# Optimization experiments

Hardware: AMD Instinct MI355X
Metric: run time of the kernel (lower is better)

## Reference

```python
import jax, jax.numpy as jnp
import numpy as np

H = 16          # num_heads
EPS = 1e-6      # RMSNorm eps


def setup_inputs() -> dict:
    key = jax.random.key(0)
    ks = jax.random.split(key, 5)
    B, N, D = 4, 4096, 1024
    x = jax.random.normal(ks[0], (B, N, D), dtype=jnp.float32)
    q = jax.random.normal(ks[1], (D,), dtype=jnp.float32)
    k = jax.random.normal(ks[2], (D,), dtype=jnp.float32)
    log_decay = jax.random.normal(ks[3], (H,), dtype=jnp.float32)
    norm_weight = jnp.ones((D,), dtype=jnp.float32)
    o_w = jax.random.normal(ks[4], (D, D), dtype=jnp.float32) * 0.02
    return {"x": x, "q": q, "k": k, "log_decay": log_decay,
            "norm_weight": norm_weight, "o_w": o_w}


def reference(x, q, k, log_decay, norm_weight, o_w):
    b, n, dm = x.shape
    dh = dm // H
    qh = q.reshape(H, dh)            # per-head query vector (constant over b, n)
    kh = k.reshape(H, dh)            # per-head key vector
    v = x.reshape(b, n, H, dh)       # values = input tokens
    # exp(logsigmoid(a)) == sigmoid(a): per-head decay in (0, 1)
    lam = jax.nn.sigmoid(log_decay)  # (H,)

    def step(S, v_t):
        # S: (b, H, dh, dh) recurrent state;  v_t: (b, H, dh)
        S = lam[None, :, None, None] * S + kh[None, :, :, None] * v_t[:, :, None, :]
        o_t = jnp.einsum('hd,bhdv->bhv', qh, S)
        return S, o_t

    S0 = jnp.zeros((b, H, dh, dh), dtype=x.dtype)
    _, o = jax.lax.scan(step, S0, jnp.moveaxis(v, 1, 0))  # o: (n, b, H, dh)
    o = jnp.moveaxis(o, 0, 1).reshape(b, n, dm)

    # RMSNorm over the channel dim
    o = o * jax.lax.rsqrt(jnp.mean(o * o, axis=-1, keepdims=True) + EPS) * norm_weight
    # o_proj (no bias)
    return o @ o_w.T
```

## Files before the change

kernel.cpp:

```cpp
#include <hip/hip_runtime.h>
#include <hip/hip_bf16.h>
#include <cstdint>
#include <cstddef>

#define HH   16
#define BB   4
#define NN   4096
#define DD   1024
#define MM   (BB * NN)
#define NC   128
#define LC   32
#define EPSV 1e-6f

typedef short short8 __attribute__((ext_vector_type(8)));
typedef float floatx4 __attribute__((ext_vector_type(4)));

__device__ __forceinline__ void async_copy16(const void* g, void* l) {
    __builtin_amdgcn_global_load_lds(
        (const __attribute__((address_space(1))) void*)g,
        (__attribute__((address_space(3))) void*)l, 16, 0, 0);
}

__device__ __forceinline__ uint2 pack_bf16x4(float a, float b, float c, float d) {
    union { __hip_bfloat16 h[4]; uint2 u; } cv;
    cv.h[0] = __float2bfloat16(a); cv.h[1] = __float2bfloat16(b);
    cv.h[2] = __float2bfloat16(c); cv.h[3] = __float2bfloat16(d);
    return cv.u;
}

__device__ __forceinline__ float sigmoidf(float a) {
    return 1.f / (1.f + expf(-a));
}

__global__ void k_wconv(const float* __restrict__ ow, const float* __restrict__ nw,
                        __hip_bfloat16* __restrict__ wp) {
    size_t i4 = (size_t)blockIdx.x * 256 + threadIdx.x;
    int j = (int)((i4 * 4) & (DD - 1));
    float4 v = ((const float4*)ow)[i4];
    ((uint2*)wp)[i4] = pack_bf16x4(v.x * nw[j], v.y * nw[j + 1],
                                   v.z * nw[j + 2], v.w * nw[j + 3]);
}

__global__ void k_chunk_end(const float* __restrict__ x, const float* __restrict__ ld,
                            float* __restrict__ E) {
    int b = blockIdx.x >> 7, c = blockIdx.x & (NC - 1);
    int j4 = threadIdx.x;
    float lam = sigmoidf(ld[j4 >> 4]);
    const float4* xp = (const float4*)(x + ((size_t)(b * NN + c * LC)) * DD) + j4;
    float4 e = {0.f, 0.f, 0.f, 0.f};
    #pragma unroll
    for (int t = 0; t < LC; ++t) {
        float4 v = xp[(size_t)t * (DD / 4)];
        e.x = fmaf(lam, e.x, v.x); e.y = fmaf(lam, e.y, v.y);
        e.z = fmaf(lam, e.z, v.z); e.w = fmaf(lam, e.w, v.w);
    }
    ((float4*)(E + (size_t)blockIdx.x * DD))[j4] = e;
}

__global__ void k_carry(const float* __restrict__ ld, const float* __restrict__ E,
                        float* __restrict__ P) {
    __shared__ float tile[NC][33];
    int b = blockIdx.x >> 5, jg = blockIdx.x & 31;
    int tid = threadIdx.x;
    int cc = tid >> 5, jj = tid & 31;
    #pragma unroll
    for (int it = 0; it < 16; ++it) {
        int c = it * 8 + cc;
        tile[c][jj] = E[(size_t)(b * NC + c) * DD + jg * 32 + jj];
    }
    __syncthreads();
    if (tid < 32) {
        int j = jg * 32 + tid;
        float lam = sigmoidf(ld[j >> 6]);
        float lamL = lam;
        lamL *= lamL; lamL *= lamL; lamL *= lamL; lamL *= lamL; lamL *= lamL;
        float p = 0.f;
        for (int c = 0; c < NC; ++c) {
            float e = tile[c][tid];
            tile[c][tid] = p;
            p = fmaf(lamL, p, e);
        }
    }
    __syncthreads();
    #pragma unroll
    for (int it = 0; it < 16; ++it) {
        int c = it * 8 + cc;
        P[(size_t)(b * NC + c) * DD + jg * 32 + jj] = tile[c][jj];
    }
}

__global__ void k_scan(const float* __restrict__ x, const float* __restrict__ q,
                       const float* __restrict__ k, const float* __restrict__ ld,
                       const float* __restrict__ P, __hip_bfloat16* __restrict__ obf,
                       float* __restrict__ sumsq) {
    __shared__ float ssq[4][LC];
    int b = blockIdx.x >> 7, c = blockIdx.x & (NC - 1);
    int j4 = threadIdx.x;
    int h = j4 >> 4;
    float lam = sigmoidf(ld[h]);
    float4 q4 = ((const float4*)q)[j4];
    float4 k4 = ((const float4*)k)[j4];
    float ch = q4.x * k4.x + q4.y * k4.y + q4.z * k4.z + q4.w * k4.w;
    #pragma unroll
    for (int off = 1; off < 16; off <<= 1) ch += __shfl_xor(ch, off);
    int row0 = b * NN + c * LC;
    int lane = threadIdx.x & 63, w = threadIdx.x >> 6;
    const float4* xp = (const float4*)(x + (size_t)row0 * DD) + j4;
    float4 y = ((const float4*)(P + (size_t)blockIdx.x * DD))[j4];
    for (int t = 0; t < LC; ++t) {
        float4 v = xp[(size_t)t * (DD / 4)];
        y.x = fmaf(lam, y.x, v.x); y.y = fmaf(lam, y.y, v.y);
        y.z = fmaf(lam, y.z, v.z); y.w = fmaf(lam, y.w, v.w);
        float ox = ch * y.x, oy = ch * y.y, oz = ch * y.z, ow = ch * y.w;
        ((uint2*)(obf + (size_t)(row0 + t) * DD))[j4] = pack_bf16x4(ox, oy, oz, ow);
        float s = ox * ox + oy * oy + oz * oz + ow * ow;
        #pragma unroll
        for (int off = 32; off > 0; off >>= 1) s += __shfl_xor(s, off);
        if (lane == 0) ssq[w][t] = s;
    }
    __syncthreads();
    if (threadIdx.x < LC) {
        int t = threadIdx.x;
        sumsq[row0 + t] = ssq[0][t] + ssq[1][t] + ssq[2][t] + ssq[3][t];
    }
}

#define GEMM_STAGE(SLOT, S)                                                    \
  do {                                                                         \
    char* _da = (char*)&lds[SLOT][0][0] + w * 1024;                            \
    char* _db = (char*)&lds[SLOT][1][0] + w * 1024;                            \
    _Pragma("unroll") for (int _i = 0; _i < 2; ++_i)                           \
      async_copy16(Ag + (size_t)(m0 + _i * 128 + rr) * 1024 + (S) * 32 + oo * 8, \
                   _da + _i * 8192);                                           \
    _Pragma("unroll") for (int _i = 0; _i < 2; ++_i)                           \
      async_copy16(Wg + (size_t)(n0 + _i * 128 + rr) * 1024 + (S) * 32 + oo * 8, \
                   _db + _i * 8192);                                           \
  } while (0)

#define GEMM_CONSUME(SLOT)                                                     \
  do {                                                                         \
    short8 af[8]; short8 bf[4];                                                \
    const short* _a = &lds[SLOT][0][0];                                        \
    const short* _b = &lds[SLOT][1][0];                                        \
    _Pragma("unroll") for (int mt = 0; mt < 8; ++mt)                           \
      af[mt] = *(const short8*)(_a + (arow_base + mt * 16) * 32 + p_rd * 8);   \
    _Pragma("unroll") for (int nt = 0; nt < 4; ++nt)                           \
      bf[nt] = *(const short8*)(_b + (brow_base + nt * 16) * 32 + p_rd * 8);   \
    asm volatile("s_waitcnt lgkmcnt(0)" ::: "memory");                         \
    __builtin_amdgcn_s_setprio(1);                                             \
    _Pragma("unroll") for (int mt = 0; mt < 8; ++mt) {                         \
      _Pragma("unroll") for (int nt = 0; nt < 4; ++nt)                         \
        acc[mt][nt] = __builtin_amdgcn_mfma_f32_16x16x32_bf16(                 \
            af[mt], bf[nt], acc[mt][nt], 0, 0, 0);                             \
    }                                                                          \
    __builtin_amdgcn_s_setprio(0);                                             \
  } while (0)

__launch_bounds__(512, 2)
__global__ void k_gemm(const __hip_bfloat16* __restrict__ A,
                       const __hip_bfloat16* __restrict__ W,
                       const float* __restrict__ sumsq, float* __restrict__ out) {
    __shared__ __attribute__((aligned(16))) short lds[4][2][256 * 32];
    const int tid = threadIdx.x;
    const int lane = tid & 63, w = tid >> 6;
    const int wm = w >> 2, wn = w & 3;
    const int g = blockIdx.x;
    const int xcd = g & 7, idx = g >> 3;
    const int bm = xcd * 8 + (idx >> 2);
    const int bn = idx & 3;
    const int m0 = bm * 256, n0 = bn * 256;
    const short* Ag = (const short*)A;
    const short* Wg = (const short*)W;

    const int rr = tid >> 2;
    const int oo = (tid & 3) ^ ((rr >> 1) & 3);

    const int p_rd = (lane >> 4) ^ (((lane & 15) >> 1) & 3);
    const int arow_base = wm * 128 + (lane & 15);
    const int brow_base = wn * 64 + (lane & 15);

    floatx4 acc[8][4] = {};

    GEMM_STAGE(0, 0); GEMM_STAGE(1, 1); GEMM_STAGE(2, 2);

    for (int s = 0; s < 29; ++s) {
        asm volatile("s_waitcnt vmcnt(8)" ::: "memory");
        __builtin_amdgcn_s_barrier();
        GEMM_STAGE((s + 3) & 3, s + 3);
        GEMM_CONSUME(s & 3);
    }
    asm volatile("s_waitcnt vmcnt(8)" ::: "memory");
    __builtin_amdgcn_s_barrier();
    GEMM_CONSUME(1);
    asm volatile("s_waitcnt vmcnt(4)" ::: "memory");
    __builtin_amdgcn_s_barrier();
    GEMM_CONSUME(2);
    asm volatile("s_waitcnt vmcnt(0)" ::: "memory");
    __builtin_amdgcn_s_barrier();
    GEMM_CONSUME(3);

    #pragma unroll
    for (int mt = 0; mt < 8; ++mt) {
        #pragma unroll
        for (int r = 0; r < 4; ++r) {
            int mrow = m0 + wm * 128 + mt * 16 + (lane >> 4) * 4 + r;
            float rs = rsqrtf(sumsq[mrow] * (1.f / 1024.f) + EPSV);
            #pragma unroll
            for (int nt = 0; nt < 4; ++nt) {
                int col = n0 + wn * 64 + nt * 16 + (lane & 15);
                out[(size_t)mrow * 1024 + col] = acc[mt][nt][r] * rs;
            }
        }
    }
}

extern "C" void kernel_launch(void* const* d_in, const int* in_sizes, int n_in,
                              void* d_out, int out_size, void* d_ws, size_t ws_size,
                              hipStream_t stream) {
    const float* x  = (const float*)d_in[0];
    const float* q  = (const float*)d_in[1];
    const float* k  = (const float*)d_in[2];
    const float* ld = (const float*)d_in[3];
    const float* nw = (const float*)d_in[4];
    const float* ow = (const float*)d_in[5];
    float* out = (float*)d_out;

    char* ws = (char*)d_ws;
    float* sumsq = (float*)(ws + 256);
    float* E     = (float*)(ws + 65792);
    float* P     = (float*)(ws + 2162944);
    __hip_bfloat16* Wp  = (__hip_bfloat16*)(ws + 4260096);
    __hip_bfloat16* Obf = (__hip_bfloat16*)(ws + 6357248);

    k_wconv<<<(DD * DD / 4) / 256, 256, 0, stream>>>(ow, nw, Wp);
    k_chunk_end<<<BB * NC, 256, 0, stream>>>(x, ld, E);
    k_carry<<<BB * 32, 256, 0, stream>>>(ld, E, P);
    k_scan<<<BB * NC, 256, 0, stream>>>(x, q, k, ld, P, Obf, sumsq);
    k_gemm<<<(MM / 256) * (DD / 256), 512, 0, stream>>>(Obf, Wp, sumsq, out);
}
```

Baseline: 174.3 us.

## Split GEMM main loop into two barrier-synchronized phases interleaving loads and MFMAs

Restructures the bf16 GEMM main loop so that each K-step runs in two phases. Each phase issues half the LDS fragment reads and half the async global-to-LDS stage copies, then a block barrier, then 16 MFMAs. This is a ping-pong style schedule meant to spread memory issue across the MFMA work and cut register pressure (af shrinks from 8 to 4 fragments). In exchange it adds extra barriers per iteration and forces the loop not to unroll.

```diff
diff --git a/kernel.cpp b/kernel.cpp
--- a/kernel.cpp
+++ b/kernel.cpp
@@ -125,33 +125,56 @@
     }
 }
 
-#define GEMM_STAGE(SLOT, S)                                                    \
+#define GEMM_STAGE_A(SLOT, S)                                                  \
   do {                                                                         \
     char* _da = (char*)&lds[SLOT][0][0] + w * 1024;                            \
-    char* _db = (char*)&lds[SLOT][1][0] + w * 1024;                            \
     _Pragma("unroll") for (int _i = 0; _i < 2; ++_i)                           \
       async_copy16(Ag + (size_t)(m0 + _i * 128 + rr) * 1024 + (S) * 32 + oo * 8, \
                    _da + _i * 8192);                                           \
+  } while (0)
+
+#define GEMM_STAGE_B(SLOT, S)                                                  \
+  do {                                                                         \
+    char* _db = (char*)&lds[SLOT][1][0] + w * 1024;                            \
     _Pragma("unroll") for (int _i = 0; _i < 2; ++_i)                           \
       async_copy16(Wg + (size_t)(n0 + _i * 128 + rr) * 1024 + (S) * 32 + oo * 8, \
                    _db + _i * 8192);                                           \
   } while (0)
 
-#define GEMM_CONSUME(SLOT)                                                     \
-  do {                                                                         \
-    short8 af[8]; short8 bf[4];                                                \
+#define PHASE_A(SLOT, DO_STAGE, S3)                                            \
+  do {                                                                         \
     const short* _a = &lds[SLOT][0][0];                                        \
     const short* _b = &lds[SLOT][1][0];                                        \
-    _Pragma("unroll") for (int mt = 0; mt < 8; ++mt)                           \
-      af[mt] = *(const short8*)(_a + (arow_base + mt * 16) * 32 + p_rd * 8);   \
     _Pragma("unroll") for (int nt = 0; nt < 4; ++nt)                           \
       bf[nt] = *(const short8*)(_b + (brow_base + nt * 16) * 32 + p_rd * 8);   \
+    _Pragma("unroll") for (int mt = 0; mt < 4; ++mt)                           \
+      af[mt] = *(const short8*)(_a + (arow_base + mt * 16) * 32 + p_rd * 8);   \
+    if (DO_STAGE) GEMM_STAGE_A((S3) & 3, S3);                                  \
+    __builtin_amdgcn_s_barrier();                                              \
     asm volatile("s_waitcnt lgkmcnt(0)" ::: "memory");                         \
     __builtin_amdgcn_s_setprio(1);                                             \
-    _Pragma("unroll") for (int mt = 0; mt < 8; ++mt) {                         \
+    _Pragma("unroll") for (int mt = 0; mt < 4; ++mt) {                         \
       _Pragma("unroll") for (int nt = 0; nt < 4; ++nt)                         \
         acc[mt][nt] = __builtin_amdgcn_mfma_f32_16x16x32_bf16(                 \
             af[mt], bf[nt], acc[mt][nt], 0, 0, 0);                             \
+    }                                                                          \
+    __builtin_amdgcn_s_setprio(0);                                             \
+    __builtin_amdgcn_s_barrier();                                              \
+  } while (0)
+
+#define PHASE_B(SLOT, DO_STAGE, S3)                                            \
+  do {                                                                         \
+    const short* _a = &lds[SLOT][0][0];                                        \
+    _Pragma("unroll") for (int mt = 0; mt < 4; ++mt)                           \
+      af[mt] = *(const short8*)(_a + (arow_base + 64 + mt * 16) * 32 + p_rd * 8); \
+    if (DO_STAGE) GEMM_STAGE_B((S3) & 3, S3);                                  \
+    __builtin_amdgcn_s_barrier();                                              \
+    asm volatile("s_waitcnt lgkmcnt(0)" ::: "memory");                         \
+    __builtin_amdgcn_s_setprio(1);                                             \
+    _Pragma("unroll") for (int mt = 0; mt < 4; ++mt) {                         \
+      _Pragma("unroll") for (int nt = 0; nt < 4; ++nt)                         \
+        acc[4 + mt][nt] = __builtin_amdgcn_mfma_f32_16x16x32_bf16(             \
+            af[mt], bf[nt], acc[4 + mt][nt], 0, 0, 0);                         \
     }                                                                          \
     __builtin_amdgcn_s_setprio(0);                                             \
   } while (0)
@@ -180,24 +203,28 @@
     const int brow_base = wn * 64 + (lane & 15);
 
     floatx4 acc[8][4] = {};
-
-    GEMM_STAGE(0, 0); GEMM_STAGE(1, 1); GEMM_STAGE(2, 2);
-
+    short8 af[4], bf[4];
+
+    GEMM_STAGE_A(0, 0); GEMM_STAGE_B(0, 0);
+    GEMM_STAGE_A(1, 1); GEMM_STAGE_B(1, 1);
+    GEMM_STAGE_A(2, 2); GEMM_STAGE_B(2, 2);
+    asm volatile("s_waitcnt vmcnt(8)" ::: "memory");
+    __builtin_amdgcn_s_barrier();
+
+    #pragma unroll 1
     for (int s = 0; s < 29; ++s) {
+        PHASE_A(s & 3, 1, s + 3);
+        PHASE_B(s & 3, 1, s + 3);
         asm volatile("s_waitcnt vmcnt(8)" ::: "memory");
         __builtin_amdgcn_s_barrier();
-        GEMM_STAGE((s + 3) & 3, s + 3);
-        GEMM_CONSUME(s & 3);
-    }
-    asm volatile("s_waitcnt vmcnt(8)" ::: "memory");
-    __builtin_amdgcn_s_barrier();
-    GEMM_CONSUME(1);
+    }
+    PHASE_A(1, 0, 0); PHASE_B(1, 0, 0);
     asm volatile("s_waitcnt vmcnt(4)" ::: "memory");
     __builtin_amdgcn_s_barrier();
-    GEMM_CONSUME(2);
+    PHASE_A(2, 0, 0); PHASE_B(2, 0, 0);
     asm volatile("s_waitcnt vmcnt(0)" ::: "memory");
     __builtin_amdgcn_s_barrier();
-    GEMM_CONSUME(3);
+    PHASE_A(3, 0, 0); PHASE_B(3, 0, 0);
 
     #pragma unroll
     for (int mt = 0; mt < 8; ++mt) {
```

After: 175.5 us. About the same (+0.7%).
